# Performance work log

Measured on AMD Instinct MI355X. Metric: run time of the kernel, lower is better.

## Reference

```python
import jax, jax.numpy as jnp
import numpy as np

B, S, D, H, DH, L, F, V, C = 2, 1024, 512, 8, 64, 8, 2048, 32000, 4

def _cond_ln(x, g_tab, b_tab, cond):
    # ConditionalLayerNorm: standard LN, scale/shift looked up per class label
    mu = jnp.mean(x, axis=-1, keepdims=True)
    var = jnp.var(x, axis=-1, keepdims=True)
    xn = (x - mu) / jnp.sqrt(var + 1e-5)
    return xn * g_tab[cond][:, None, :] + b_tab[cond][:, None, :]

def _rot_half(t):
    t1, t2 = jnp.split(t, 2, axis=-1)
    return jnp.concatenate([-t2, t1], axis=-1)

def setup_inputs():
    key = jax.random.key(0)
    ks = jax.random.split(key, 24)
    def p(k, shape, s=0.02):
        return (jax.random.normal(k, shape) * s).astype(jnp.float32)
    return {
        'inputs': jax.random.randint(ks[0], (B, S), 0, V, dtype=jnp.int32),
        'cond': jax.random.randint(ks[1], (B,), 0, C, dtype=jnp.int32),
        'input_mask': jnp.ones((B, S), jnp.float32),
        'inverse_temperature': 1,
        'embedding': p(ks[2], (V, D), 0.1),
        'pos_emb': p(ks[3], (S, D)),
        'Wq': p(ks[4], (L, D, D)), 'bq': jnp.zeros((L, D), jnp.float32),
        'Wk': p(ks[5], (L, D, D)), 'bk': jnp.zeros((L, D), jnp.float32),
        'Wv': p(ks[6], (L, D, D)), 'bv': jnp.zeros((L, D), jnp.float32),
        'Wo': p(ks[7], (L, D, D)), 'bo': jnp.zeros((L, D), jnp.float32),
        'W1': p(ks[8], (L, D, F)), 'b1': jnp.zeros((L, F), jnp.float32),
        'W2': p(ks[9], (L, F, D)), 'b2': jnp.zeros((L, D), jnp.float32),
        'cn1_g': jnp.ones((L, C, D), jnp.float32) + p(ks[10], (L, C, D), 0.01),
        'cn1_b': p(ks[11], (L, C, D), 0.01),
        'cn2_g': jnp.ones((L, C, D), jnp.float32) + p(ks[12], (L, C, D), 0.01),
        'cn2_b': p(ks[13], (L, C, D), 0.01),
        'norm_g': jnp.ones((C, D), jnp.float32) + p(ks[14], (C, D), 0.01),
        'norm_b': p(ks[15], (C, D), 0.01),
        'Wout': p(ks[16], (D, V), 0.05),
        'bout': jnp.zeros((V,), jnp.float32),
    }

def _logits(inputs, cond, input_mask, embedding, pos_emb, Wq, bq, Wk, bk, Wv, bv,
            Wo, bo, W1, b1, W2, b2, cn1_g, cn1_b, cn2_g, cn2_b, norm_g, norm_b, Wout, bout):
    b, s = inputs.shape
    x = embedding[inputs] + pos_emb[None, :s]  # [B,S,D]; dropout = identity (eval)
    # rotary tables for head dim DH
    inv_freq = 1.0 / (10000.0 ** (jnp.arange(0, DH, 2, dtype=jnp.float32) / DH))
    freqs = jnp.arange(s, dtype=jnp.float32)[:, None] * inv_freq
    emb = jnp.concatenate([freqs, freqs], axis=-1)
    cos = jnp.cos(emb)[None, :, None, :]
    sin = jnp.sin(emb)[None, :, None, :]
    kmask = input_mask[:, :, None, None]  # LengthMask applied to keys
    for l in range(L):
        q = (x @ Wq[l] + bq[l]).reshape(b, s, H, DH)
        k = (x @ Wk[l] + bk[l]).reshape(b, s, H, DH)
        v = (x @ Wv[l] + bv[l]).reshape(b, s, H, DH)
        q = q * cos + _rot_half(q) * sin
        k = k * cos + _rot_half(k) * sin
        # causal linear attention: phi = elu + 1, prefix-sum KV state
        q = jax.nn.elu(q) + 1.0
        k = (jax.nn.elu(k) + 1.0) * kmask
        kv = jnp.cumsum(k[..., :, None] * v[..., None, :], axis=1)  # [B,S,H,DH,DH]
        z = jnp.cumsum(k, axis=1)                                   # [B,S,H,DH]
        num = jnp.einsum('bshd,bshde->bshe', q, kv)
        den = jnp.einsum('bshd,bshd->bsh', q, z) + 1e-6
        a = (num / den[..., None]).reshape(b, s, D)
        # post-norm encoder layer (fast-transformers layout) with conditional LN
        x = x + a @ Wo[l] + bo[l]
        x = _cond_ln(x, cn1_g[l], cn1_b[l], cond)
        y = jax.nn.gelu(x @ W1[l] + b1[l]) @ W2[l] + b2[l]
        x = _cond_ln(x + y, cn2_g[l], cn2_b[l], cond)
    x = _cond_ln(x, norm_g, norm_b, cond)
    return x @ Wout + bout

def reference(inputs, cond, input_mask, inverse_temperature, embedding, pos_emb,
              Wq, bq, Wk, bk, Wv, bv, Wo, bo, W1, b1, W2, b2,
              cn1_g, cn1_b, cn2_g, cn2_b, norm_g, norm_b, Wout, bout):
    out = _logits(inputs, cond, input_mask, embedding, pos_emb, Wq, bq, Wk, bk, Wv, bv,
                  Wo, bo, W1, b1, W2, b2, cn1_g, cn1_b, cn2_g, cn2_b, norm_g, norm_b, Wout, bout)
    # straight-through gumbel softmax
    g = jax.random.gumbel(jax.random.key(42), out.shape, out.dtype)
    it = jnp.asarray(inverse_temperature, out.dtype)
    y = jax.nn.softmax((out + g) * it, axis=-1)
    y1 = jax.nn.one_hot(jnp.argmax(y, axis=-1), out.shape[-1], dtype=y.dtype)
    out_gumbel = jax.lax.stop_gradient(y1 - y) + y
    return out, out_gumbel
```

## Files before the change

kernel.cpp:

```cpp
#include <hip/hip_runtime.h>
#include <math.h>

#define DD 512
#define SS 1024
#define BB 2
#define HH 8
#define LL 8
#define FF 2048
#define VV 32000
#define ROWS 2048
#define NTOT 65536000u
#define NCHUNK 16
#define CLEN 64

__global__ __launch_bounds__(256) void embed_kernel(
    const int* __restrict__ ids, const float* __restrict__ emb,
    const float* __restrict__ pos, float* __restrict__ x)
{
    unsigned idx = blockIdx.x * 256u + threadIdx.x;
    unsigned row = idx >> 9, d = idx & 511u;
    unsigned s = row & (SS - 1);
    x[idx] = emb[(size_t)ids[row] * DD + d] + pos[(size_t)s * DD + d];
}

__global__ __launch_bounds__(256) void rope_table_kernel(float* __restrict__ ctab,
                                                         float* __restrict__ stab)
{
    unsigned idx = blockIdx.x * 256u + threadIdx.x;
    unsigned j = idx & 31u, s = idx >> 5;
    float invf = (float)(1.0 / pow(10000.0, (double)(2 * j) / 64.0));
    float f = (float)s * invf;
    ctab[idx] = (float)cos((double)f);
    stab[idx] = (float)sin((double)f);
}

__device__ __forceinline__ float elu1(float x) {
    return x > 0.f ? x + 1.f : expm1f(x) + 1.f;
}

__global__ __launch_bounds__(256) void rope_feat_kernel(
    float* __restrict__ q, float* __restrict__ k,
    const float* __restrict__ ctab, const float* __restrict__ stab,
    const float* __restrict__ mask)
{
    unsigned idx = blockIdx.x * 256u + threadIdx.x;
    unsigned j = idx & 31u;
    unsigned h = (idx >> 5) & 7u;
    unsigned row = idx >> 8;
    unsigned s = row & (SS - 1);
    float c = ctab[s * 32 + j], sn = stab[s * 32 + j];
    size_t o = (size_t)row * DD + h * 64 + j;
    float q1 = q[o], q2 = q[o + 32];
    float qa = q1 * c - q2 * sn;
    float qb = q2 * c + q1 * sn;
    q[o]      = elu1(qa);
    q[o + 32] = elu1(qb);
    float m = mask[row];
    float k1 = k[o], k2 = k[o + 32];
    float ka = k1 * c - k2 * sn;
    float kb = k2 * c + k1 * sn;
    k[o]      = elu1(ka) * m;
    k[o + 32] = elu1(kb) * m;
}

__global__ __launch_bounds__(256) void chunk_state_kernel(
    const float* __restrict__ k, const float* __restrict__ v,
    float* __restrict__ st, float* __restrict__ zs)
{
    int blk = blockIdx.x;
    int bh = blk >> 4, c = blk & 15;
    int b = bh >> 3, h = bh & 7;
    int t = threadIdx.x;
    int e = t & 63, dg = t >> 6, d0 = dg << 4;
    size_t base = (size_t)b * SS * DD + (size_t)h * 64 + (size_t)(c * CLEN) * DD;
    __shared__ float kk[64][64], vv[64][64];
#pragma unroll
    for (int i = 0; i < 4; ++i) {
        int idx = t + i * 256;
        int r = idx >> 4, c4 = (idx & 15) << 2;
        size_t go = base + (size_t)r * DD + c4;
        *(float4*)&kk[r][c4] = *(const float4*)(k + go);
        *(float4*)&vv[r][c4] = *(const float4*)(v + go);
    }
    __syncthreads();
    float acc[16];
#pragma unroll
    for (int j = 0; j < 16; ++j) acc[j] = 0.f;
    float z = 0.f;
    for (int s = 0; s < CLEN; ++s) {
        float vval = vv[s][e];
        float kr16[16];
        *(float4*)&kr16[0]  = *(const float4*)&kk[s][d0];
        *(float4*)&kr16[4]  = *(const float4*)&kk[s][d0 + 4];
        *(float4*)&kr16[8]  = *(const float4*)&kk[s][d0 + 8];
        *(float4*)&kr16[12] = *(const float4*)&kk[s][d0 + 12];
#pragma unroll
        for (int j = 0; j < 16; ++j) acc[j] += kr16[j] * vval;
        if (t < 64) z += kk[s][t];
    }
    size_t so = (size_t)blk * 4096;
#pragma unroll
    for (int j = 0; j < 16; ++j)
        st[so + (size_t)(d0 + j) * 64 + e] = acc[j];
    if (t < 64) zs[(size_t)blk * 64 + t] = z;
}

__global__ __launch_bounds__(256) void chunk_prefix_kernel(
    float* __restrict__ st, float* __restrict__ zs)
{
    int bh = blockIdx.x;
    int t = threadIdx.x;
    float run[16];
#pragma unroll
    for (int i = 0; i < 16; ++i) run[i] = 0.f;
    float zrun = 0.f;
    for (int c = 0; c < NCHUNK; ++c) {
        size_t so = ((size_t)bh * NCHUNK + c) * 4096;
#pragma unroll
        for (int i = 0; i < 16; ++i) {
            size_t o = so + t + i * 256;
            float tmp = st[o];
            st[o] = run[i];
            run[i] += tmp;
        }
        if (t < 64) {
            size_t zo = ((size_t)bh * NCHUNK + c) * 64 + t;
            float tz = zs[zo];
            zs[zo] = zrun;
            zrun += tz;
        }
    }
}

__global__ __launch_bounds__(256) void chunk_scan_kernel(
    const float* __restrict__ q, const float* __restrict__ k,
    const float* __restrict__ v, float* __restrict__ a,
    const float* __restrict__ st, const float* __restrict__ zs)
{
    int blk = blockIdx.x;
    int bh = blk >> 4, c = blk & 15;
    int b = bh >> 3, h = bh & 7;
    int t = threadIdx.x;
    int e = t & 63, dg = t >> 6, d0 = dg << 4;
    size_t base = (size_t)b * SS * DD + (size_t)h * 64 + (size_t)(c * CLEN) * DD;
    __shared__ float kk[64][64], vv[64][64], qq[64][64];
    __shared__ float pnum[4][64];
    __shared__ float den_sh;
#pragma unroll
    for (int i = 0; i < 4; ++i) {
        int idx = t + i * 256;
        int r = idx >> 4, c4 = (idx & 15) << 2;
        size_t go = base + (size_t)r * DD + c4;
        *(float4*)&kk[r][c4] = *(const float4*)(k + go);
        *(float4*)&vv[r][c4] = *(const float4*)(v + go);
        *(float4*)&qq[r][c4] = *(const float4*)(q + go);
    }
    float Sacc[16];
    size_t so = (size_t)blk * 4096;
#pragma unroll
    for (int j = 0; j < 16; ++j)
        Sacc[j] = st[so + (size_t)(d0 + j) * 64 + e];
    float zreg = 0.f;
    if (t < 64) zreg = zs[(size_t)blk * 64 + t];
    __syncthreads();
    for (int s = 0; s < CLEN; ++s) {
        float vval = vv[s][e];
        float kr16[16], qr16[16];
        *(float4*)&kr16[0]  = *(const float4*)&kk[s][d0];
        *(float4*)&kr16[4]  = *(const float4*)&kk[s][d0 + 4];
        *(float4*)&kr16[8]  = *(const float4*)&kk[s][d0 + 8];
        *(float4*)&kr16[12] = *(const float4*)&kk[s][d0 + 12];
        *(float4*)&qr16[0]  = *(const float4*)&qq[s][d0];
        *(float4*)&qr16[4]  = *(const float4*)&qq[s][d0 + 4];
        *(float4*)&qr16[8]  = *(const float4*)&qq[s][d0 + 8];
        *(float4*)&qr16[12] = *(const float4*)&qq[s][d0 + 12];
        float p = 0.f;
#pragma unroll
        for (int j = 0; j < 16; ++j) {
            Sacc[j] += kr16[j] * vval;
            p += qr16[j] * Sacc[j];
        }
        pnum[dg][e] = p;
        if (t < 64) {
            zreg += kk[s][t];
            float pd = qq[s][t] * zreg;
#pragma unroll
            for (int o = 32; o; o >>= 1) pd += __shfl_down(pd, o);
            if (t == 0) den_sh = pd + 1e-6f;
        }
        __syncthreads();
        if (t < 64) {
            float num = ((pnum[0][t] + pnum[1][t]) + pnum[2][t]) + pnum[3][t];
            a[base + (size_t)s * DD + t] = num / den_sh;
        }
        __syncthreads();
    }
}

__global__ __launch_bounds__(256) void gemm_kernel(
    const float* __restrict__ A, const float* __restrict__ B,
    const float* __restrict__ bias, const float* __restrict__ res,
    float* __restrict__ C, int M, int N, int K, int act)
{
    __shared__ float As[16][68];
    __shared__ float Bs[16][68];
    const int t = threadIdx.x;
    const int bn = blockIdx.x, bm = blockIdx.y;
    const int m0 = bm * 64, n0 = bn * 64;
    const int tx = t & 15, ty = t >> 4;
    const int ar = t >> 2, ac = (t & 3) << 2;
    const int br = t >> 4, bc = (t & 15) << 2;
    const float* Ap = A + (size_t)(m0 + ar) * K + ac;
    const float* Bp = B + (size_t)br * N + (n0 + bc);
    float4 av = *(const float4*)(Ap);
    float4 bv = *(const float4*)(Bp);
    float acc[4][4] = {};
    for (int k0 = 0; k0 < K; k0 += 16) {
        As[ac + 0][ar] = av.x; As[ac + 1][ar] = av.y;
        As[ac + 2][ar] = av.z; As[ac + 3][ar] = av.w;
        *(float4*)&Bs[br][bc] = bv;
        __syncthreads();
        if (k0 + 16 < K) {
            av = *(const float4*)(Ap + k0 + 16);
            bv = *(const float4*)(Bp + (size_t)(k0 + 16) * N);
        }
#pragma unroll
        for (int kkk = 0; kkk < 16; ++kkk) {
            float4 a4 = *(const float4*)&As[kkk][ty << 2];
            float4 b4 = *(const float4*)&Bs[kkk][tx << 2];
            float aa[4] = {a4.x, a4.y, a4.z, a4.w};
            float bb4[4] = {b4.x, b4.y, b4.z, b4.w};
#pragma unroll
            for (int i = 0; i < 4; ++i)
#pragma unroll
                for (int jj = 0; jj < 4; ++jj)
                    acc[i][jj] += aa[i] * bb4[jj];
        }
        __syncthreads();
    }
#pragma unroll
    for (int i = 0; i < 4; ++i) {
        int m = m0 + (ty << 2) + i;
        size_t rowoff = (size_t)m * N + n0 + (tx << 2);
        float tmp[4];
#pragma unroll
        for (int jj = 0; jj < 4; ++jj) {
            int n = n0 + (tx << 2) + jj;
            float vv = acc[i][jj] + bias[n];
            if (res) vv += res[rowoff + jj];
            if (act == 1) {
                float x3 = vv * vv * vv;
                vv = vv * (0.5f * (1.0f + tanhf(0.7978845608028654f * (vv + 0.044715f * x3))));
            }
            tmp[jj] = vv;
        }
        float4 o4 = {tmp[0], tmp[1], tmp[2], tmp[3]};
        *(float4*)(C + rowoff) = o4;
    }
}

#define PAD128 132
__global__ __launch_bounds__(256) void gemm128_kernel(
    const float* __restrict__ A, const float* __restrict__ B,
    const float* __restrict__ bias, const float* __restrict__ res,
    float* __restrict__ C, int M, int N, int K, int act)
{
    __shared__ float As[16][PAD128];
    __shared__ float Bs[16][PAD128];
    const int t = threadIdx.x;
    const int bn = blockIdx.x, bm = blockIdx.y;
    const int m0 = bm * 128, n0 = bn * 128;
    const int tx = t & 15, ty = t >> 4;
    const int ar = t >> 2, ac = (t & 3) << 2;
    const int br = t >> 5, bc = (t & 31) << 2;
    const float* Ap0 = A + (size_t)(m0 + ar) * K + ac;
    const float* Ap1 = A + (size_t)(m0 + 64 + ar) * K + ac;
    const float* Bp0 = B + (size_t)br * N + (n0 + bc);
    const float* Bp1 = B + (size_t)(br + 8) * N + (n0 + bc);
    float4 a0 = *(const float4*)(Ap0);
    float4 a1 = *(const float4*)(Ap1);
    float4 b0 = *(const float4*)(Bp0);
    float4 b1 = *(const float4*)(Bp1);
    float acc[8][8] = {};
    for (int k0 = 0; k0 < K; k0 += 16) {
        As[ac + 0][ar] = a0.x; As[ac + 1][ar] = a0.y;
        As[ac + 2][ar] = a0.z; As[ac + 3][ar] = a0.w;
        As[ac + 0][64 + ar] = a1.x; As[ac + 1][64 + ar] = a1.y;
        As[ac + 2][64 + ar] = a1.z; As[ac + 3][64 + ar] = a1.w;
        *(float4*)&Bs[br][bc] = b0;
        *(float4*)&Bs[br + 8][bc] = b1;
        __syncthreads();
        if (k0 + 16 < K) {
            a0 = *(const float4*)(Ap0 + k0 + 16);
            a1 = *(const float4*)(Ap1 + k0 + 16);
            b0 = *(const float4*)(Bp0 + (size_t)(k0 + 16) * N);
            b1 = *(const float4*)(Bp1 + (size_t)(k0 + 16) * N);
        }
#pragma unroll
        for (int kkk = 0; kkk < 16; ++kkk) {
            float4 aA = *(const float4*)&As[kkk][ty << 2];
            float4 aB = *(const float4*)&As[kkk][64 + (ty << 2)];
            float4 bA = *(const float4*)&Bs[kkk][tx << 2];
            float4 bB = *(const float4*)&Bs[kkk][64 + (tx << 2)];
            float am[8] = {aA.x, aA.y, aA.z, aA.w, aB.x, aB.y, aB.z, aB.w};
            float bn8[8] = {bA.x, bA.y, bA.z, bA.w, bB.x, bB.y, bB.z, bB.w};
#pragma unroll
            for (int i = 0; i < 8; ++i)
#pragma unroll
                for (int jj = 0; jj < 8; ++jj)
                    acc[i][jj] += am[i] * bn8[jj];
        }
        __syncthreads();
    }
#pragma unroll
    for (int i = 0; i < 8; ++i) {
        int m = m0 + ((i >> 2) << 6) + (ty << 2) + (i & 3);
#pragma unroll
        for (int nh = 0; nh < 2; ++nh) {
            int nb = n0 + (nh << 6) + (tx << 2);
            size_t off = (size_t)m * N + nb;
            float tmp[4];
#pragma unroll
            for (int jj = 0; jj < 4; ++jj) {
                float vv2 = acc[i][(nh << 2) + jj] + bias[nb + jj];
                if (res) vv2 += res[off + jj];
                if (act == 1) {
                    float x3 = vv2 * vv2 * vv2;
                    vv2 = vv2 * (0.5f * (1.0f + tanhf(0.7978845608028654f * (vv2 + 0.044715f * x3))));
                }
                tmp[jj] = vv2;
            }
            float4 o4 = {tmp[0], tmp[1], tmp[2], tmp[3]};
            *(float4*)(C + off) = o4;
        }
    }
}

__global__ __launch_bounds__(256) void ln_kernel(
    const float* __restrict__ in, float* __restrict__ out,
    const float* __restrict__ g, const float* __restrict__ b,
    const int* __restrict__ cond)
{
    int row = blockIdx.x;
    int c = cond[row >> 10];
    const float* xr = in + (size_t)row * DD;
    int t = threadIdx.x;
    float v0 = xr[t], v1 = xr[t + 256];
    __shared__ float sm[8];
    int lane = t & 63, w = t >> 6;
    float s1 = v0 + v1;
#pragma unroll
    for (int o = 32; o; o >>= 1) s1 += __shfl_down(s1, o);
    if (lane == 0) sm[w] = s1;
    __syncthreads();
    if (t == 0) sm[0] = sm[0] + sm[1] + sm[2] + sm[3];
    __syncthreads();
    float mu = sm[0] * (1.0f / 512.0f);
    __syncthreads();
    float d0 = v0 - mu, d1 = v1 - mu;
    float s2 = d0 * d0 + d1 * d1;
#pragma unroll
    for (int o = 32; o; o >>= 1) s2 += __shfl_down(s2, o);
    if (lane == 0) sm[w] = s2;
    __syncthreads();
    if (t == 0) sm[0] = sm[0] + sm[1] + sm[2] + sm[3];
    __syncthreads();
    float var = sm[0] * (1.0f / 512.0f);
    float sd = sqrtf(var + 1e-5f);
    const float* gr = g + (size_t)c * DD;
    const float* br = b + (size_t)c * DD;
    out[(size_t)row * DD + t]       = (d0 / sd) * gr[t] + br[t];
    out[(size_t)row * DD + t + 256] = (d1 / sd) * gr[t + 256] + br[t + 256];
}

__device__ __forceinline__ unsigned rotl32(unsigned x, int r) {
    return (x << r) | (x >> (32 - r));
}

__device__ __forceinline__ float gumbel_noise(unsigned i)
{
    const unsigned k0 = 0u, k1 = 42u, k2 = 0x1BD11BDAu ^ 0u ^ 42u;
    unsigned x0 = 0u;
    unsigned x1 = i;
#define TFR(r) { x0 += x1; x1 = rotl32(x1, r); x1 ^= x0; }
    x0 += k0; x1 += k1;
    TFR(13) TFR(15) TFR(26) TFR(6)
    x0 += k1; x1 += k2 + 1u;
    TFR(17) TFR(29) TFR(16) TFR(24)
    x0 += k2; x1 += k0 + 2u;
    TFR(13) TFR(15) TFR(26) TFR(6)
    x0 += k0; x1 += k1 + 3u;
    TFR(17) TFR(29) TFR(16) TFR(24)
    x0 += k1; x1 += k2 + 4u;
    TFR(13) TFR(15) TFR(26) TFR(6)
    x0 += k2; x1 += k0 + 5u;
#undef TFR
    unsigned bits = x0 ^ x1;
    float u = __uint_as_float((bits >> 9) | 0x3f800000u) - 1.0f;
    float uu = u > 0.f ? u : 1.175494350822288e-38f;
    return -logf(-logf(uu));
}

__global__ __launch_bounds__(256) void gumbel_argmax_kernel(
    const float* __restrict__ logits, float* __restrict__ out1)
{
    int row = blockIdx.x;
    unsigned base = (unsigned)row * VV;
    int t = threadIdx.x;
    float best = -3.4e38f;
    int bi = VV;
    for (int v = t; v < VV; v += 256) {
        float val = logits[base + v] + gumbel_noise(base + v);
        if (val > best) { best = val; bi = v; }
    }
    __shared__ float bv[256];
    __shared__ int bix[256];
    bv[t] = best; bix[t] = bi;
    __syncthreads();
    for (int off = 128; off; off >>= 1) {
        if (t < off) {
            float ov = bv[t + off]; int oi = bix[t + off];
            if (ov > bv[t] || (ov == bv[t] && oi < bix[t])) { bv[t] = ov; bix[t] = oi; }
        }
        __syncthreads();
    }
    int amax = bix[0];
    for (int v = t; v < VV; v += 256)
        out1[base + v] = (v == amax) ? 1.0f : 0.0f;
}

extern "C" void kernel_launch(void* const* d_in, const int* in_sizes, int n_in,
                              void* d_out, int out_size, void* d_ws, size_t ws_size,
                              hipStream_t stream)
{
    const int*   ids   = (const int*)  d_in[0];
    const int*   cond  = (const int*)  d_in[1];
    const float* mask  = (const float*)d_in[2];
    const float* emb   = (const float*)d_in[4];
    const float* pos   = (const float*)d_in[5];
    const float* Wq    = (const float*)d_in[6];
    const float* bq    = (const float*)d_in[7];
    const float* Wk    = (const float*)d_in[8];
    const float* bk    = (const float*)d_in[9];
    const float* Wv    = (const float*)d_in[10];
    const float* bv    = (const float*)d_in[11];
    const float* Wo    = (const float*)d_in[12];
    const float* bo    = (const float*)d_in[13];
    const float* W1    = (const float*)d_in[14];
    const float* b1    = (const float*)d_in[15];
    const float* W2    = (const float*)d_in[16];
    const float* b2    = (const float*)d_in[17];
    const float* cn1g  = (const float*)d_in[18];
    const float* cn1b  = (const float*)d_in[19];
    const float* cn2g  = (const float*)d_in[20];
    const float* cn2b  = (const float*)d_in[21];
    const float* ng    = (const float*)d_in[22];
    const float* nb    = (const float*)d_in[23];
    const float* Wout  = (const float*)d_in[24];
    const float* bout  = (const float*)d_in[25];

    float* out0 = (float*)d_out;
    float* out1 = out0 + (size_t)NTOT;

    const size_t NX = (size_t)ROWS * DD;
    float* ws   = (float*)d_ws;
    float* x    = ws;
    float* xr   = x + NX;
    float* qb   = xr + NX;
    float* kb   = qb + NX;
    float* vb2  = kb + NX;
    float* ab   = vb2 + NX;
    float* h1   = ab + NX;
    float* ctab = h1 + (size_t)ROWS * FF;
    float* stab = ctab + SS * 32;

    float* stbuf = h1;
    float* zbuf  = h1 + (size_t)BB * HH * NCHUNK * 4096;

    embed_kernel<<<(ROWS * DD) / 256, 256, 0, stream>>>(ids, emb, pos, x);
    rope_table_kernel<<<(SS * 32) / 256, 256, 0, stream>>>(ctab, stab);

    for (int l = 0; l < LL; ++l) {
        const float* wq = Wq + (size_t)l * DD * DD;
        const float* wk = Wk + (size_t)l * DD * DD;
        const float* wv = Wv + (size_t)l * DD * DD;
        const float* wo = Wo + (size_t)l * DD * DD;
        const float* w1 = W1 + (size_t)l * DD * FF;
        const float* w2 = W2 + (size_t)l * FF * DD;

        dim3 g512(DD / 64, ROWS / 64);
        gemm_kernel<<<g512, 256, 0, stream>>>(x, wq, bq + l * DD, nullptr, qb, ROWS, DD, DD, 0);
        gemm_kernel<<<g512, 256, 0, stream>>>(x, wk, bk + l * DD, nullptr, kb, ROWS, DD, DD, 0);
        gemm_kernel<<<g512, 256, 0, stream>>>(x, wv, bv + l * DD, nullptr, vb2, ROWS, DD, DD, 0);

        rope_feat_kernel<<<(ROWS * HH * 32) / 256, 256, 0, stream>>>(qb, kb, ctab, stab, mask);

        chunk_state_kernel<<<BB * HH * NCHUNK, 256, 0, stream>>>(kb, vb2, stbuf, zbuf);
        chunk_prefix_kernel<<<BB * HH, 256, 0, stream>>>(stbuf, zbuf);
        chunk_scan_kernel<<<BB * HH * NCHUNK, 256, 0, stream>>>(qb, kb, vb2, ab, stbuf, zbuf);

        gemm_kernel<<<g512, 256, 0, stream>>>(ab, wo, bo + l * DD, x, xr, ROWS, DD, DD, 0);
        ln_kernel<<<ROWS, 256, 0, stream>>>(xr, x, cn1g + (size_t)l * 4 * DD, cn1b + (size_t)l * 4 * DD, cond);

        dim3 g128f(FF / 128, ROWS / 128);
        gemm128_kernel<<<g128f, 256, 0, stream>>>(x, w1, b1 + l * FF, nullptr, h1, ROWS, FF, DD, 1);
        gemm_kernel<<<dim3(DD / 64, ROWS / 64), 256, 0, stream>>>(h1, w2, b2 + l * DD, x, xr, ROWS, DD, FF, 0);
        ln_kernel<<<ROWS, 256, 0, stream>>>(xr, x, cn2g + (size_t)l * 4 * DD, cn2b + (size_t)l * 4 * DD, cond);
    }

    ln_kernel<<<ROWS, 256, 0, stream>>>(x, xr, ng, nb, cond);

    dim3 gV128(VV / 128, ROWS / 128);
    gemm128_kernel<<<gV128, 256, 0, stream>>>(xr, Wout, bout, nullptr, out0, ROWS, VV, DD, 0);

    gumbel_argmax_kernel<<<ROWS, 256, 0, stream>>>(out0, out1);
}
```

Baseline: 4.135 ms.

## Fuse QKV and rope into attention, double-buffer GEMMs, split-K with fused LN

Merges the three QKV projections into one launch and folds the rotary/ELU feature map into the chunk state and scan kernels, removing the separate rope pass. Adds double-buffered shared memory to all GEMMs, plus block swizzling in the 128 GEMM. Wo and W2 now run as split-K GEMMs whose two partials are summed with bias and residual inside a new fused LayerNorm kernel. W1 switches from the 128-tile GEMM to the 64-tile GEMM. Split-K writes partial buffers that reuse the q/k storage; rope is recomputed for K in both attention kernels.

```diff
diff --git a/kernel.cpp b/kernel.cpp
--- a/kernel.cpp
+++ b/kernel.cpp
@@ -38,33 +38,10 @@
     return x > 0.f ? x + 1.f : expm1f(x) + 1.f;
 }
 
-__global__ __launch_bounds__(256) void rope_feat_kernel(
-    float* __restrict__ q, float* __restrict__ k,
-    const float* __restrict__ ctab, const float* __restrict__ stab,
-    const float* __restrict__ mask)
-{
-    unsigned idx = blockIdx.x * 256u + threadIdx.x;
-    unsigned j = idx & 31u;
-    unsigned h = (idx >> 5) & 7u;
-    unsigned row = idx >> 8;
-    unsigned s = row & (SS - 1);
-    float c = ctab[s * 32 + j], sn = stab[s * 32 + j];
-    size_t o = (size_t)row * DD + h * 64 + j;
-    float q1 = q[o], q2 = q[o + 32];
-    float qa = q1 * c - q2 * sn;
-    float qb = q2 * c + q1 * sn;
-    q[o]      = elu1(qa);
-    q[o + 32] = elu1(qb);
-    float m = mask[row];
-    float k1 = k[o], k2 = k[o + 32];
-    float ka = k1 * c - k2 * sn;
-    float kb = k2 * c + k1 * sn;
-    k[o]      = elu1(ka) * m;
-    k[o + 32] = elu1(kb) * m;
-}
-
 __global__ __launch_bounds__(256) void chunk_state_kernel(
     const float* __restrict__ k, const float* __restrict__ v,
+    const float* __restrict__ ctab, const float* __restrict__ stab,
+    const float* __restrict__ mask,
     float* __restrict__ st, float* __restrict__ zs)
 {
     int blk = blockIdx.x;
@@ -81,6 +58,18 @@
         size_t go = base + (size_t)r * DD + c4;
         *(float4*)&kk[r][c4] = *(const float4*)(k + go);
         *(float4*)&vv[r][c4] = *(const float4*)(v + go);
+    }
+    __syncthreads();
+#pragma unroll
+    for (int i = 0; i < 8; ++i) {
+        int idx = t + (i << 8);
+        int r = idx >> 5, j = idx & 31;
+        int s = c * CLEN + r;
+        float cc = ctab[s * 32 + j], sn = stab[s * 32 + j];
+        float m = mask[b * SS + s];
+        float k1 = kk[r][j], k2 = kk[r][j + 32];
+        kk[r][j]      = elu1(k1 * cc - k2 * sn) * m;
+        kk[r][j + 32] = elu1(k2 * cc + k1 * sn) * m;
     }
     __syncthreads();
     float acc[16];
@@ -135,6 +124,8 @@
 __global__ __launch_bounds__(256) void chunk_scan_kernel(
     const float* __restrict__ q, const float* __restrict__ k,
     const float* __restrict__ v, float* __restrict__ a,
+    const float* __restrict__ ctab, const float* __restrict__ stab,
+    const float* __restrict__ mask,
     const float* __restrict__ st, const float* __restrict__ zs)
 {
     int blk = blockIdx.x;
@@ -154,6 +145,21 @@
         *(float4*)&kk[r][c4] = *(const float4*)(k + go);
         *(float4*)&vv[r][c4] = *(const float4*)(v + go);
         *(float4*)&qq[r][c4] = *(const float4*)(q + go);
+    }
+    __syncthreads();
+#pragma unroll
+    for (int i = 0; i < 8; ++i) {
+        int idx = t + (i << 8);
+        int r = idx >> 5, j = idx & 31;
+        int s = c * CLEN + r;
+        float cc = ctab[s * 32 + j], sn = stab[s * 32 + j];
+        float m = mask[b * SS + s];
+        float k1 = kk[r][j], k2 = kk[r][j + 32];
+        kk[r][j]      = elu1(k1 * cc - k2 * sn) * m;
+        kk[r][j + 32] = elu1(k2 * cc + k1 * sn) * m;
+        float q1 = qq[r][j], q2 = qq[r][j + 32];
+        qq[r][j]      = elu1(q1 * cc - q2 * sn);
+        qq[r][j + 32] = elu1(q2 * cc + q1 * sn);
     }
     float Sacc[16];
     size_t so = (size_t)blk * 4096;
@@ -202,8 +208,8 @@
     const float* __restrict__ bias, const float* __restrict__ res,
     float* __restrict__ C, int M, int N, int K, int act)
 {
-    __shared__ float As[16][68];
-    __shared__ float Bs[16][68];
+    __shared__ float As[2][16][68];
+    __shared__ float Bs[2][16][68];
     const int t = threadIdx.x;
     const int bn = blockIdx.x, bm = blockIdx.y;
     const int m0 = bm * 64, n0 = bn * 64;
@@ -214,20 +220,24 @@
     const float* Bp = B + (size_t)br * N + (n0 + bc);
     float4 av = *(const float4*)(Ap);
     float4 bv = *(const float4*)(Bp);
+    As[0][ac + 0][ar] = av.x; As[0][ac + 1][ar] = av.y;
+    As[0][ac + 2][ar] = av.z; As[0][ac + 3][ar] = av.w;
+    *(float4*)&Bs[0][br][bc] = bv;
+    __syncthreads();
     float acc[4][4] = {};
-    for (int k0 = 0; k0 < K; k0 += 16) {
-        As[ac + 0][ar] = av.x; As[ac + 1][ar] = av.y;
-        As[ac + 2][ar] = av.z; As[ac + 3][ar] = av.w;
-        *(float4*)&Bs[br][bc] = bv;
-        __syncthreads();
-        if (k0 + 16 < K) {
-            av = *(const float4*)(Ap + k0 + 16);
-            bv = *(const float4*)(Bp + (size_t)(k0 + 16) * N);
+    const int nt = K >> 4;
+    for (int it = 0; it < nt; ++it) {
+        const int cur = it & 1;
+        const bool more = (it + 1) < nt;
+        float4 av2, bv2;
+        if (more) {
+            av2 = *(const float4*)(Ap + ((it + 1) << 4));
+            bv2 = *(const float4*)(Bp + (size_t)((it + 1) << 4) * N);
         }
 #pragma unroll
         for (int kkk = 0; kkk < 16; ++kkk) {
-            float4 a4 = *(const float4*)&As[kkk][ty << 2];
-            float4 b4 = *(const float4*)&Bs[kkk][tx << 2];
+            float4 a4 = *(const float4*)&As[cur][kkk][ty << 2];
+            float4 b4 = *(const float4*)&Bs[cur][kkk][tx << 2];
             float aa[4] = {a4.x, a4.y, a4.z, a4.w};
             float bb4[4] = {b4.x, b4.y, b4.z, b4.w};
 #pragma unroll
@@ -236,7 +246,12 @@
                 for (int jj = 0; jj < 4; ++jj)
                     acc[i][jj] += aa[i] * bb4[jj];
         }
-        __syncthreads();
+        if (more) {
+            As[cur ^ 1][ac + 0][ar] = av2.x; As[cur ^ 1][ac + 1][ar] = av2.y;
+            As[cur ^ 1][ac + 2][ar] = av2.z; As[cur ^ 1][ac + 3][ar] = av2.w;
+            *(float4*)&Bs[cur ^ 1][br][bc] = bv2;
+            __syncthreads();
+        }
     }
 #pragma unroll
     for (int i = 0; i < 4; ++i) {
@@ -259,16 +274,152 @@
     }
 }
 
+__global__ __launch_bounds__(256) void qkv_kernel(
+    const float* __restrict__ A,
+    const float* __restrict__ Wq, const float* __restrict__ Wk, const float* __restrict__ Wv,
+    const float* __restrict__ bq, const float* __restrict__ bk, const float* __restrict__ bv,
+    float* __restrict__ Qo, float* __restrict__ Ko, float* __restrict__ Vo)
+{
+    __shared__ float As[2][16][68];
+    __shared__ float Bs[2][16][68];
+    const int t = threadIdx.x;
+    const int bn = blockIdx.x, bm = blockIdx.y;
+    const int sel = bn >> 3;
+    const float* B    = sel == 0 ? Wq : (sel == 1 ? Wk : Wv);
+    const float* bias = sel == 0 ? bq : (sel == 1 ? bk : bv);
+    float*       C    = sel == 0 ? Qo : (sel == 1 ? Ko : Vo);
+    const int m0 = bm * 64, n0 = (bn & 7) << 6;
+    const int tx = t & 15, ty = t >> 4;
+    const int ar = t >> 2, ac = (t & 3) << 2;
+    const int br = t >> 4, bc = (t & 15) << 2;
+    const float* Ap = A + (size_t)(m0 + ar) * DD + ac;
+    const float* Bp = B + (size_t)br * DD + (n0 + bc);
+    float4 av = *(const float4*)(Ap);
+    float4 bv4 = *(const float4*)(Bp);
+    As[0][ac + 0][ar] = av.x; As[0][ac + 1][ar] = av.y;
+    As[0][ac + 2][ar] = av.z; As[0][ac + 3][ar] = av.w;
+    *(float4*)&Bs[0][br][bc] = bv4;
+    __syncthreads();
+    float acc[4][4] = {};
+    const int nt = DD >> 4;
+    for (int it = 0; it < nt; ++it) {
+        const int cur = it & 1;
+        const bool more = (it + 1) < nt;
+        float4 av2, bv2;
+        if (more) {
+            av2 = *(const float4*)(Ap + ((it + 1) << 4));
+            bv2 = *(const float4*)(Bp + (size_t)((it + 1) << 4) * DD);
+        }
+#pragma unroll
+        for (int kkk = 0; kkk < 16; ++kkk) {
+            float4 a4 = *(const float4*)&As[cur][kkk][ty << 2];
+            float4 b4 = *(const float4*)&Bs[cur][kkk][tx << 2];
+            float aa[4] = {a4.x, a4.y, a4.z, a4.w};
+            float bb4[4] = {b4.x, b4.y, b4.z, b4.w};
+#pragma unroll
+            for (int i = 0; i < 4; ++i)
+#pragma unroll
+                for (int jj = 0; jj < 4; ++jj)
+                    acc[i][jj] += aa[i] * bb4[jj];
+        }
+        if (more) {
+            As[cur ^ 1][ac + 0][ar] = av2.x; As[cur ^ 1][ac + 1][ar] = av2.y;
+            As[cur ^ 1][ac + 2][ar] = av2.z; As[cur ^ 1][ac + 3][ar] = av2.w;
+            *(float4*)&Bs[cur ^ 1][br][bc] = bv2;
+            __syncthreads();
+        }
+    }
+#pragma unroll
+    for (int i = 0; i < 4; ++i) {
+        int m = m0 + (ty << 2) + i;
+        size_t rowoff = (size_t)m * DD + n0 + (tx << 2);
+        float4 o4;
+        o4.x = acc[i][0] + bias[n0 + (tx << 2) + 0];
+        o4.y = acc[i][1] + bias[n0 + (tx << 2) + 1];
+        o4.z = acc[i][2] + bias[n0 + (tx << 2) + 2];
+        o4.w = acc[i][3] + bias[n0 + (tx << 2) + 3];
+        *(float4*)(C + rowoff) = o4;
+    }
+}
+
+__global__ __launch_bounds__(256) void gemm_splitk_kernel(
+    const float* __restrict__ A, const float* __restrict__ B,
+    float* __restrict__ C, int M, int N, int K)
+{
+    __shared__ float As[2][16][68];
+    __shared__ float Bs[2][16][68];
+    const int t = threadIdx.x;
+    const int bn = blockIdx.x, bm = blockIdx.y, ks = blockIdx.z;
+    const int Kc = K >> 1;
+    const int m0 = bm * 64, n0 = bn * 64;
+    const int tx = t & 15, ty = t >> 4;
+    const int ar = t >> 2, ac = (t & 3) << 2;
+    const int br = t >> 4, bc = (t & 15) << 2;
+    const float* Ap = A + (size_t)(m0 + ar) * K + ks * Kc + ac;
+    const float* Bp = B + (size_t)(ks * Kc + br) * N + (n0 + bc);
+    float4 av = *(const float4*)(Ap);
+    float4 bv = *(const float4*)(Bp);
+    As[0][ac + 0][ar] = av.x; As[0][ac + 1][ar] = av.y;
+    As[0][ac + 2][ar] = av.z; As[0][ac + 3][ar] = av.w;
+    *(float4*)&Bs[0][br][bc] = bv;
+    __syncthreads();
+    float acc[4][4] = {};
+    const int nt = Kc >> 4;
+    for (int it = 0; it < nt; ++it) {
+        const int cur = it & 1;
+        const bool more = (it + 1) < nt;
+        float4 av2, bv2;
+        if (more) {
+            av2 = *(const float4*)(Ap + ((it + 1) << 4));
+            bv2 = *(const float4*)(Bp + (size_t)((it + 1) << 4) * N);
+        }
+#pragma unroll
+        for (int kkk = 0; kkk < 16; ++kkk) {
+            float4 a4 = *(const float4*)&As[cur][kkk][ty << 2];
+            float4 b4 = *(const float4*)&Bs[cur][kkk][tx << 2];
+            float aa[4] = {a4.x, a4.y, a4.z, a4.w};
+            float bb4[4] = {b4.x, b4.y, b4.z, b4.w};
+#pragma unroll
+            for (int i = 0; i < 4; ++i)
+#pragma unroll
+                for (int jj = 0; jj < 4; ++jj)
+                    acc[i][jj] += aa[i] * bb4[jj];
+        }
+        if (more) {
+            As[cur ^ 1][ac + 0][ar] = av2.x; As[cur ^ 1][ac + 1][ar] = av2.y;
+            As[cur ^ 1][ac + 2][ar] = av2.z; As[cur ^ 1][ac + 3][ar] = av2.w;
+            *(float4*)&Bs[cur ^ 1][br][bc] = bv2;
+            __syncthreads();
+        }
+    }
+    float* Cp = C + (size_t)ks * M * N;
+#pragma unroll
+    for (int i = 0; i < 4; ++i) {
+        int m = m0 + (ty << 2) + i;
+        size_t rowoff = (size_t)m * N + n0 + (tx << 2);
+        float4 o4 = {acc[i][0], acc[i][1], acc[i][2], acc[i][3]};
+        *(float4*)(Cp + rowoff) = o4;
+    }
+}
+
 #define PAD128 132
 __global__ __launch_bounds__(256) void gemm128_kernel(
     const float* __restrict__ A, const float* __restrict__ B,
     const float* __restrict__ bias, const float* __restrict__ res,
     float* __restrict__ C, int M, int N, int K, int act)
 {
-    __shared__ float As[16][PAD128];
-    __shared__ float Bs[16][PAD128];
+    __shared__ float As[2][16][PAD128];
+    __shared__ float Bs[2][16][PAD128];
     const int t = threadIdx.x;
-    const int bn = blockIdx.x, bm = blockIdx.y;
+    unsigned p = blockIdx.y * gridDim.x + blockIdx.x;
+    unsigned total = gridDim.x * gridDim.y;
+    unsigned bn, bm;
+    if ((total & 7u) == 0u) {
+        unsigned per = total >> 3;
+        unsigned virt = (p & 7u) * per + (p >> 3);
+        bm = virt % gridDim.y;
+        bn = virt / gridDim.y;
+    } else { bn = blockIdx.x; bm = blockIdx.y; }
     const int m0 = bm * 128, n0 = bn * 128;
     const int tx = t & 15, ty = t >> 4;
     const int ar = t >> 2, ac = (t & 3) << 2;
@@ -281,27 +432,32 @@
     float4 a1 = *(const float4*)(Ap1);
     float4 b0 = *(const float4*)(Bp0);
     float4 b1 = *(const float4*)(Bp1);
+    As[0][ac + 0][ar] = a0.x; As[0][ac + 1][ar] = a0.y;
+    As[0][ac + 2][ar] = a0.z; As[0][ac + 3][ar] = a0.w;
+    As[0][ac + 0][64 + ar] = a1.x; As[0][ac + 1][64 + ar] = a1.y;
+    As[0][ac + 2][64 + ar] = a1.z; As[0][ac + 3][64 + ar] = a1.w;
+    *(float4*)&Bs[0][br][bc] = b0;
+    *(float4*)&Bs[0][br + 8][bc] = b1;
+    __syncthreads();
     float acc[8][8] = {};
-    for (int k0 = 0; k0 < K; k0 += 16) {
-        As[ac + 0][ar] = a0.x; As[ac + 1][ar] = a0.y;
-        As[ac + 2][ar] = a0.z; As[ac + 3][ar] = a0.w;
-        As[ac + 0][64 + ar] = a1.x; As[ac + 1][64 + ar] = a1.y;
-        As[ac + 2][64 + ar] = a1.z; As[ac + 3][64 + ar] = a1.w;
-        *(float4*)&Bs[br][bc] = b0;
-        *(float4*)&Bs[br + 8][bc] = b1;
-        __syncthreads();
-        if (k0 + 16 < K) {
-            a0 = *(const float4*)(Ap0 + k0 + 16);
-            a1 = *(const float4*)(Ap1 + k0 + 16);
-            b0 = *(const float4*)(Bp0 + (size_t)(k0 + 16) * N);
-            b1 = *(const float4*)(Bp1 + (size_t)(k0 + 16) * N);
+    const int nt = K >> 4;
+    for (int it = 0; it < nt; ++it) {
+        const int cur = it & 1;
+        const bool more = (it + 1) < nt;
+        float4 a0n, a1n, b0n, b1n;
+        if (more) {
+            int ko = (it + 1) << 4;
+            a0n = *(const float4*)(Ap0 + ko);
+            a1n = *(const float4*)(Ap1 + ko);
+            b0n = *(const float4*)(Bp0 + (size_t)ko * N);
+            b1n = *(const float4*)(Bp1 + (size_t)ko * N);
         }
 #pragma unroll
         for (int kkk = 0; kkk < 16; ++kkk) {
-            float4 aA = *(const float4*)&As[kkk][ty << 2];
-            float4 aB = *(const float4*)&As[kkk][64 + (ty << 2)];
-            float4 bA = *(const float4*)&Bs[kkk][tx << 2];
-            float4 bB = *(const float4*)&Bs[kkk][64 + (tx << 2)];
+            float4 aA = *(const float4*)&As[cur][kkk][ty << 2];
+            float4 aB = *(const float4*)&As[cur][kkk][64 + (ty << 2)];
+            float4 bA = *(const float4*)&Bs[cur][kkk][tx << 2];
+            float4 bB = *(const float4*)&Bs[cur][kkk][64 + (tx << 2)];
             float am[8] = {aA.x, aA.y, aA.z, aA.w, aB.x, aB.y, aB.z, aB.w};
             float bn8[8] = {bA.x, bA.y, bA.z, bA.w, bB.x, bB.y, bB.z, bB.w};
 #pragma unroll
@@ -310,7 +466,15 @@
                 for (int jj = 0; jj < 8; ++jj)
                     acc[i][jj] += am[i] * bn8[jj];
         }
-        __syncthreads();
+        if (more) {
+            As[cur ^ 1][ac + 0][ar] = a0n.x; As[cur ^ 1][ac + 1][ar] = a0n.y;
+            As[cur ^ 1][ac + 2][ar] = a0n.z; As[cur ^ 1][ac + 3][ar] = a0n.w;
+            As[cur ^ 1][ac + 0][64 + ar] = a1n.x; As[cur ^ 1][ac + 1][64 + ar] = a1n.y;
+            As[cur ^ 1][ac + 2][64 + ar] = a1n.z; As[cur ^ 1][ac + 3][64 + ar] = a1n.w;
+            *(float4*)&Bs[cur ^ 1][br][bc] = b0n;
+            *(float4*)&Bs[cur ^ 1][br + 8][bc] = b1n;
+            __syncthreads();
+        }
     }
 #pragma unroll
     for (int i = 0; i < 8; ++i) {
@@ -371,6 +535,45 @@
     const float* br = b + (size_t)c * DD;
     out[(size_t)row * DD + t]       = (d0 / sd) * gr[t] + br[t];
     out[(size_t)row * DD + t + 256] = (d1 / sd) * gr[t + 256] + br[t + 256];
+}
+
+__global__ __launch_bounds__(256) void ln_fuse_kernel(
+    const float* __restrict__ p0, const float* __restrict__ p1,
+    const float* __restrict__ bias, float* __restrict__ x,
+    const float* __restrict__ g, const float* __restrict__ b,
+    const int* __restrict__ cond)
+{
+    int row = blockIdx.x;
+    int c = cond[row >> 10];
+    int t = threadIdx.x;
+    size_t o0 = (size_t)row * DD + t, o1 = o0 + 256;
+    float v0 = p0[o0] + p1[o0] + bias[t]       + x[o0];
+    float v1 = p0[o1] + p1[o1] + bias[t + 256] + x[o1];
+    __shared__ float sm[8];
+    int lane = t & 63, w = t >> 6;
+    float s1 = v0 + v1;
+#pragma unroll
+    for (int o = 32; o; o >>= 1) s1 += __shfl_down(s1, o);
+    if (lane == 0) sm[w] = s1;
+    __syncthreads();
+    if (t == 0) sm[0] = sm[0] + sm[1] + sm[2] + sm[3];
+    __syncthreads();
+    float mu = sm[0] * (1.0f / 512.0f);
+    __syncthreads();
+    float d0 = v0 - mu, d1 = v1 - mu;
+    float s2 = d0 * d0 + d1 * d1;
+#pragma unroll
+    for (int o = 32; o; o >>= 1) s2 += __shfl_down(s2, o);
+    if (lane == 0) sm[w] = s2;
+    __syncthreads();
+    if (t == 0) sm[0] = sm[0] + sm[1] + sm[2] + sm[3];
+    __syncthreads();
+    float var = sm[0] * (1.0f / 512.0f);
+    float sd = sqrtf(var + 1e-5f);
+    const float* gr = g + (size_t)c * DD;
+    const float* br = b + (size_t)c * DD;
+    x[o0] = (d0 / sd) * gr[t]       + br[t];
+    x[o1] = (d1 / sd) * gr[t + 256] + br[t + 256];
 }
 
 __device__ __forceinline__ unsigned rotl32(unsigned x, int r) {
@@ -488,24 +691,21 @@
         const float* w1 = W1 + (size_t)l * DD * FF;
         const float* w2 = W2 + (size_t)l * FF * DD;
 
-        dim3 g512(DD / 64, ROWS / 64);
-        gemm_kernel<<<g512, 256, 0, stream>>>(x, wq, bq + l * DD, nullptr, qb, ROWS, DD, DD, 0);
-        gemm_kernel<<<g512, 256, 0, stream>>>(x, wk, bk + l * DD, nullptr, kb, ROWS, DD, DD, 0);
-        gemm_kernel<<<g512, 256, 0, stream>>>(x, wv, bv + l * DD, nullptr, vb2, ROWS, DD, DD, 0);
-
-        rope_feat_kernel<<<(ROWS * HH * 32) / 256, 256, 0, stream>>>(qb, kb, ctab, stab, mask);
-
-        chunk_state_kernel<<<BB * HH * NCHUNK, 256, 0, stream>>>(kb, vb2, stbuf, zbuf);
+        qkv_kernel<<<dim3(24, 32), 256, 0, stream>>>(
+            x, wq, wk, wv, bq + l * DD, bk + l * DD, bv + l * DD, qb, kb, vb2);
+
+        chunk_state_kernel<<<BB * HH * NCHUNK, 256, 0, stream>>>(kb, vb2, ctab, stab, mask, stbuf, zbuf);
         chunk_prefix_kernel<<<BB * HH, 256, 0, stream>>>(stbuf, zbuf);
-        chunk_scan_kernel<<<BB * HH * NCHUNK, 256, 0, stream>>>(qb, kb, vb2, ab, stbuf, zbuf);
-
-        gemm_kernel<<<g512, 256, 0, stream>>>(ab, wo, bo + l * DD, x, xr, ROWS, DD, DD, 0);
-        ln_kernel<<<ROWS, 256, 0, stream>>>(xr, x, cn1g + (size_t)l * 4 * DD, cn1b + (size_t)l * 4 * DD, cond);
-
-        dim3 g128f(FF / 128, ROWS / 128);
-        gemm128_kernel<<<g128f, 256, 0, stream>>>(x, w1, b1 + l * FF, nullptr, h1, ROWS, FF, DD, 1);
-        gemm_kernel<<<dim3(DD / 64, ROWS / 64), 256, 0, stream>>>(h1, w2, b2 + l * DD, x, xr, ROWS, DD, FF, 0);
-        ln_kernel<<<ROWS, 256, 0, stream>>>(xr, x, cn2g + (size_t)l * 4 * DD, cn2b + (size_t)l * 4 * DD, cond);
+        chunk_scan_kernel<<<BB * HH * NCHUNK, 256, 0, stream>>>(qb, kb, vb2, ab, ctab, stab, mask, stbuf, zbuf);
+
+        gemm_splitk_kernel<<<dim3(8, 32, 2), 256, 0, stream>>>(ab, wo, qb, ROWS, DD, DD);
+        ln_fuse_kernel<<<ROWS, 256, 0, stream>>>(qb, kb, bo + l * DD, x,
+                                                 cn1g + (size_t)l * 4 * DD, cn1b + (size_t)l * 4 * DD, cond);
+
+        gemm_kernel<<<dim3(FF / 64, ROWS / 64), 256, 0, stream>>>(x, w1, b1 + l * FF, nullptr, h1, ROWS, FF, DD, 1);
+        gemm_splitk_kernel<<<dim3(8, 32, 2), 256, 0, stream>>>(h1, w2, qb, ROWS, DD, FF);
+        ln_fuse_kernel<<<ROWS, 256, 0, stream>>>(qb, kb, b2 + l * DD, x,
+                                                 cn2g + (size_t)l * 4 * DD, cn2b + (size_t)l * 4 * DD, cond);
     }
 
     ln_kernel<<<ROWS, 256, 0, stream>>>(x, xr, ng, nb, cond);
```

After: 4.136 ms. About the same (+0.0%).
